# Kernel tuning notes

Measured on AMD Instinct MI355X. Metric: run time of the kernel, lower is better.

The kernel has to match this reference:

```python
import jax, jax.numpy as jnp
import numpy as np

N, E, C, NNZ, D = 100000, 50000, 2000, 1600000, 128


def _seg_mean(vals, idx, num):
    s = jax.ops.segment_sum(vals, idx, num_segments=num)
    cnt = jax.ops.segment_sum(jnp.ones((vals.shape[0],), vals.dtype), idx, num_segments=num)
    return s / jnp.maximum(cnt, 1.0)[:, None]


def _prelu(x, a):
    return jnp.where(x >= 0, x, a * x)


def setup_inputs() -> dict:
    key = jax.random.key(0)
    ks = jax.random.split(key, 32)
    x = jax.random.normal(ks[0], (N, D), jnp.float32)
    src = jax.random.randint(ks[1], (NNZ,), 0, N)
    dst = jax.random.randint(ks[2], (NNZ,), 0, E)
    hyperedge_index = jnp.stack([src, dst])
    hyperedge_component_index = jnp.stack([jnp.arange(E), jax.random.randint(ks[3], (E,), 0, C)])
    node_component_index = jnp.stack([jnp.arange(N), jax.random.randint(ks[4], (N,), 0, C)])
    inp = {
        'x': x,
        'hyperedge_index': hyperedge_index,
        'hyperedge_component_index': hyperedge_component_index,
        'node_component_index': node_component_index,
        'num_nodes': N, 'num_edges': E, 'num_components': C,
        'prelu_a': jnp.float32(0.25),
    }
    ki = 5
    for layer in range(2):
        for name in ['v2e', 'e2v', 'e2c', 'n2c']:
            inp[f'W_{name}_{layer}'] = jax.random.normal(ks[ki], (D, D), jnp.float32) / np.sqrt(D).astype(np.float32)
            inp[f'b_{name}_{layer}'] = jnp.zeros((D,), jnp.float32)
            ki += 1
    return inp


def reference(x, hyperedge_index, hyperedge_component_index, node_component_index,
              num_nodes, num_edges, num_components, prelu_a,
              W_v2e_0, b_v2e_0, W_e2v_0, b_e2v_0, W_e2c_0, b_e2c_0, W_n2c_0, b_n2c_0,
              W_v2e_1, b_v2e_1, W_e2v_1, b_e2v_1, W_e2c_1, b_e2c_1, W_n2c_1, b_n2c_1):
    Nn, Ne, Nc = num_nodes, num_edges, num_components
    # self-loop construction: node i joins fresh hyperedge Ne + i
    src = jnp.concatenate([hyperedge_index[0], jnp.arange(Nn)])
    dst = jnp.concatenate([hyperedge_index[1], jnp.arange(Ne, Ne + Nn)])
    E_tot = Ne + Nn
    he_e, he_c = hyperedge_component_index[0], hyperedge_component_index[1]
    nc_n, nc_c = node_component_index[0], node_component_index[1]

    def conv(h, Wv, bv, We, be, Wec, bec, Wnc, bnc):
        # node -> edge: transform, gather along incidences, scatter-mean to edges
        e = _prelu(_seg_mean((h @ Wv + bv)[src], dst, E_tot), prelu_a)
        # edge -> node
        n = _seg_mean((e @ We + be)[dst], src, Nn)
        # edge -> component  +  node -> component
        c = _prelu(_seg_mean((e @ Wec + bec)[he_e], he_c, Nc)
                   + _seg_mean((n @ Wnc + bnc)[nc_n], nc_c, Nc), prelu_a)
        return n, e, c

    n, e, c = conv(x, W_v2e_0, b_v2e_0, W_e2v_0, b_e2v_0, W_e2c_0, b_e2c_0, W_n2c_0, b_n2c_0)
    h = _prelu(n, prelu_a)
    n, e, c = conv(h, W_v2e_1, b_v2e_1, W_e2v_1, b_e2v_1, W_e2c_1, b_e2c_1, W_n2c_1, b_n2c_1)
    return _prelu(n, prelu_a), e[:Ne], c
```

## Files before the change

kernel.cpp:

```cpp
#include <hip/hip_runtime.h>
#include <hip/hip_bf16.h>

#define NN 100000
#define EE 50000
#define CC 2000
#define NNZ 1600000
#define DD 128
#define ET (EE + NN)

#define PB 800
#define CHUNK 2000
#define NBK 196
#define SCAP 12288

__device__ __forceinline__ float prelu(float x, float a) {
    return x >= 0.f ? x : a * x;
}

__device__ __forceinline__ float bf2f(unsigned short h) {
    return __uint_as_float(((unsigned int)h) << 16);
}
__device__ __forceinline__ unsigned short f2bf(float f) {
    unsigned int u = __float_as_uint(f);
    u = (u + 0x7fff + ((u >> 16) & 1)) >> 16;
    return (unsigned short)u;
}

struct alignas(16) us8 { ushort4 lo, hi; };

__global__ void comp_hist(const int* __restrict__ hec, const int* __restrict__ ncc,
                          int* __restrict__ c1cnt, int* __restrict__ c2cnt) {
    int i = blockIdx.x * blockDim.x + threadIdx.x;
    int stride = gridDim.x * blockDim.x;
    for (int k = i; k < EE; k += stride) atomicAdd(&c1cnt[hec[k]], 1);
    for (int k = i; k < NN; k += stride) atomicAdd(&c2cnt[ncc[k]], 1);
}

__global__ __launch_bounds__(256) void part_hist(const int* __restrict__ src,
                                                 const int* __restrict__ dst,
                                                 int* __restrict__ etot,
                                                 int* __restrict__ ntot) {
    __shared__ int he[NBK], hn[NBK];
    for (int i = threadIdx.x; i < NBK; i += 256) { he[i] = 0; hn[i] = 0; }
    __syncthreads();
    int b = blockIdx.x;
    int beg = b * CHUNK, end = min(beg + CHUNK, NNZ);
    for (int k = beg + threadIdx.x; k < end; k += 256) {
        atomicAdd(&he[dst[k] >> 8], 1);
        atomicAdd(&hn[src[k] >> 9], 1);
    }
    __syncthreads();
    for (int i = threadIdx.x; i < NBK; i += 256) {
        if (he[i]) atomicAdd(&etot[i], he[i]);
        if (hn[i]) atomicAdd(&ntot[i], hn[i]);
    }
}

__global__ __launch_bounds__(256) void scan_small(const int* __restrict__ etot,
        const int* __restrict__ ntot, int* __restrict__ ebase, int* __restrict__ nbase,
        int* __restrict__ ecur, int* __restrict__ ncur) {
    __shared__ int se[256], sn[256];
    int t = threadIdx.x;
    int ve = (t < NBK) ? etot[t] : 0;
    int vn = (t < NBK) ? ntot[t] : 0;
    se[t] = ve; sn[t] = vn;
    __syncthreads();
    for (int off = 1; off < 256; off <<= 1) {
        int ae = (t >= off) ? se[t - off] : 0;
        int an = (t >= off) ? sn[t - off] : 0;
        __syncthreads();
        se[t] += ae; sn[t] += an;
        __syncthreads();
    }
    if (t < NBK) {
        int be = se[t] - ve, bn = sn[t] - vn;
        ebase[t] = be; ecur[t] = be;
        nbase[t] = bn; ncur[t] = bn;
    }
    if (t == 0) { ebase[NBK] = NNZ; nbase[NBK] = NNZ; }
}

__global__ __launch_bounds__(256) void reorder_kernel(const int* __restrict__ src,
        const int* __restrict__ dst, int* __restrict__ ecur, int* __restrict__ ncur,
        int2* __restrict__ pe, int2* __restrict__ pn) {
    __shared__ int sS[CHUNK], sD[CHUNK];
    __shared__ int he[NBK], hn[NBK];
    __shared__ int beA[NBK], bnA[NBK];
    int b = blockIdx.x;
    int beg = b * CHUNK;
    int n = min(CHUNK, NNZ - beg);
    for (int i = threadIdx.x; i < NBK; i += 256) { he[i] = 0; hn[i] = 0; }
    for (int i = threadIdx.x; i < n; i += 256) {
        sS[i] = src[beg + i];
        sD[i] = dst[beg + i];
    }
    __syncthreads();
    for (int i = threadIdx.x; i < n; i += 256) {
        atomicAdd(&he[sD[i] >> 8], 1);
        atomicAdd(&hn[sS[i] >> 9], 1);
    }
    __syncthreads();
    for (int i = threadIdx.x; i < NBK; i += 256) {
        beA[i] = he[i] ? atomicAdd(&ecur[i], he[i]) : 0;
        bnA[i] = hn[i] ? atomicAdd(&ncur[i], hn[i]) : 0;
        he[i] = 0; hn[i] = 0;
    }
    __syncthreads();
    for (int i = threadIdx.x; i < n; i += 256) {
        int d = sD[i], s = sS[i];
        int bk = d >> 8;
        int p = beA[bk] + atomicAdd(&he[bk], 1);
        pe[p] = make_int2(d, s);
        bk = s >> 9;
        p = bnA[bk] + atomicAdd(&hn[bk], 1);
        pn[p] = make_int2(s, d);
    }
}

template <int W, int SHIFT>
__global__ __launch_bounds__(256) void bucket_scatter(const int2* __restrict__ pairs,
        const int* __restrict__ bases, int* __restrict__ ptr_excl,
        int* __restrict__ csr, int segn) {
    __shared__ int cnt[W];
    __shared__ int stage[SCAP];
    int b = blockIdx.x;
    int base = bases[b];
    int bend = bases[b + 1];
    int bsize = bend - base;

    for (int i = threadIdx.x; i < W; i += 256) cnt[i] = 0;
    __syncthreads();
    for (int k = base + threadIdx.x; k < bend; k += 256)
        atomicAdd(&cnt[pairs[k].x - (b << SHIFT)], 1);
    __syncthreads();

    int l0 = threadIdx.x, l1 = threadIdx.x + 256;
    int o0 = cnt[l0];
    int o1 = (W > 256) ? cnt[l1] : 0;
    for (int off = 1; off < W; off <<= 1) {
        int v0 = (l0 >= off) ? cnt[l0 - off] : 0;
        int v1 = 0;
        if (W > 256 && l1 >= off) v1 = cnt[l1 - off];
        __syncthreads();
        cnt[l0] += v0;
        if (W > 256) cnt[l1] += v1;
        __syncthreads();
    }
    int e0 = cnt[l0] - o0;
    int e1 = (W > 256) ? (cnt[l1] - o1) : 0;
    __syncthreads();
    cnt[l0] = base + e0;
    if (W > 256) cnt[l1] = base + e1;
    int g0 = (b << SHIFT) + l0;
    if (g0 < segn) ptr_excl[g0] = base + e0;
    if (W > 256) {
        int g1 = (b << SHIFT) + l1;
        if (g1 < segn) ptr_excl[g1] = base + e1;
    }
    if (b == NBK - 1 && threadIdx.x == 0) ptr_excl[segn] = NNZ;
    __syncthreads();

    bool fb = (bsize > SCAP);
    for (int k = base + threadIdx.x; k < bend; k += 256) {
        int2 pr = pairs[k];
        int pos = atomicAdd(&cnt[pr.x - (b << SHIFT)], 1);
        if (!fb) stage[pos - base] = pr.y;
        else     csr[pos] = pr.y;
    }
    __syncthreads();
    if (!fb)
        for (int t = threadIdx.x; t < bsize; t += 256) csr[base + t] = stage[t];
}

template <bool PRELU_IN, bool PRELU_OUT, bool OUT_BF16>
__global__ __launch_bounds__(256) void gemm128(
        const float* __restrict__ H, const float* __restrict__ W,
        const float* __restrict__ bias, void* __restrict__ outv,
        float* __restrict__ out2 ,
        const int* __restrict__ gate ,
        int M, const float* __restrict__ a_ptr) {
    __shared__ float Wl[128 * 128];
    for (int i = threadIdx.x; i < 4096; i += 256)
        ((float4*)Wl)[i] = ((const float4*)W)[i];
    float a = 0.f;
    if (PRELU_IN || PRELU_OUT) a = *a_ptr;
    __syncthreads();

    const int jc = threadIdx.x & 15;
    const int rg = threadIdx.x >> 4;
    const int j0 = jc * 8;
    const int row0 = blockIdx.x * 64 + rg * 4;

    float acc[4][8];
#pragma unroll
    for (int r = 0; r < 4; ++r)
#pragma unroll
        for (int c = 0; c < 8; ++c) acc[r][c] = 0.f;

    int rclamp[4];
#pragma unroll
    for (int r = 0; r < 4; ++r) {
        int row = row0 + r;
        rclamp[r] = row < M ? row : (M - 1);
    }

#pragma unroll 2
    for (int k0 = 0; k0 < 128; k0 += 4) {
        float hr[4][4];
#pragma unroll
        for (int r = 0; r < 4; ++r) {
            float4 v = *(const float4*)(H + (size_t)rclamp[r] * DD + k0);
            if (PRELU_IN) {
                v.x = prelu(v.x, a); v.y = prelu(v.y, a);
                v.z = prelu(v.z, a); v.w = prelu(v.w, a);
            }
            hr[r][0] = v.x; hr[r][1] = v.y; hr[r][2] = v.z; hr[r][3] = v.w;
        }
#pragma unroll
        for (int kk = 0; kk < 4; ++kk) {
            const float4 w0 = *(const float4*)&Wl[(k0 + kk) * 128 + j0];
            const float4 w1 = *(const float4*)&Wl[(k0 + kk) * 128 + j0 + 4];
#pragma unroll
            for (int r = 0; r < 4; ++r) {
                float h = hr[r][kk];
                acc[r][0] += h * w0.x; acc[r][1] += h * w0.y;
                acc[r][2] += h * w0.z; acc[r][3] += h * w0.w;
                acc[r][4] += h * w1.x; acc[r][5] += h * w1.y;
                acc[r][6] += h * w1.z; acc[r][7] += h * w1.w;
            }
        }
    }

    float bb[8];
#pragma unroll
    for (int c = 0; c < 8; ++c) bb[c] = bias[j0 + c];

#pragma unroll
    for (int r = 0; r < 4; ++r) {
        int row = row0 + r;
        if (row < M) {
            float g = 1.f;
            if (gate) g = (gate[row] > 0) ? 1.f : 0.f;
            float o[8];
#pragma unroll
            for (int c = 0; c < 8; ++c) o[c] = acc[r][c] + bb[c] * g;
            if (OUT_BF16) {
                us8 o8;
                o8.lo = make_ushort4(f2bf(o[0]), f2bf(o[1]), f2bf(o[2]), f2bf(o[3]));
                o8.hi = make_ushort4(f2bf(o[4]), f2bf(o[5]), f2bf(o[6]), f2bf(o[7]));
                *(us8*)((unsigned short*)outv + (size_t)row * DD + j0) = o8;
            } else {
                float* out = (float*)outv;
                *(float4*)(out + (size_t)row * DD + j0)     = make_float4(o[0], o[1], o[2], o[3]);
                *(float4*)(out + (size_t)row * DD + j0 + 4) = make_float4(o[4], o[5], o[6], o[7]);
            }
            if (PRELU_OUT) {
                *(float4*)(out2 + (size_t)row * DD + j0) =
                    make_float4(prelu(o[0], a), prelu(o[1], a), prelu(o[2], a), prelu(o[3], a));
                *(float4*)(out2 + (size_t)row * DD + j0 + 4) =
                    make_float4(prelu(o[4], a), prelu(o[5], a), prelu(o[6], a), prelu(o[7], a));
            }
        }
    }
}

__global__ __launch_bounds__(256) void edge_agg(const unsigned short* __restrict__ hv,
        const int* __restrict__ eptr, const int* __restrict__ ecsr,
        unsigned short* __restrict__ Eb, float* __restrict__ out_e,
        const float* __restrict__ a_ptr) {
    int j = blockIdx.x * 4 + (threadIdx.x >> 6);
    if (j >= EE) return;
    int lane = threadIdx.x & 63;
    int half = lane >> 5, l32 = lane & 31;
    int p0 = eptr[j], p1 = eptr[j + 1];
    float a = *a_ptr;
    float4 s = make_float4(0.f, 0.f, 0.f, 0.f);
    for (int p = p0 + half; p < p1; p += 2) {
        int row = ecsr[p];
        ushort4 v = *(const ushort4*)(hv + (size_t)row * DD + l32 * 4);
        s.x += bf2f(v.x); s.y += bf2f(v.y); s.z += bf2f(v.z); s.w += bf2f(v.w);
    }
    s.x += __shfl_xor(s.x, 32);
    s.y += __shfl_xor(s.y, 32);
    s.z += __shfl_xor(s.z, 32);
    s.w += __shfl_xor(s.w, 32);
    if (half == 0) {
        float inv = 1.0f / fmaxf((float)(p1 - p0), 1.0f);
        float4 o = make_float4(prelu(s.x * inv, a), prelu(s.y * inv, a),
                               prelu(s.z * inv, a), prelu(s.w * inv, a));
        *(ushort4*)(Eb + (size_t)j * DD + l32 * 4) =
            make_ushort4(f2bf(o.x), f2bf(o.y), f2bf(o.z), f2bf(o.w));
        if (out_e) *(float4*)(out_e + (size_t)j * DD + l32 * 4) = o;
    }
}

__global__ __launch_bounds__(256) void node_agg(const unsigned short* __restrict__ Eb,
        const unsigned short* __restrict__ hv, const int* __restrict__ nptr,
        const int* __restrict__ ncsr, float* __restrict__ nagg,
        const float* __restrict__ a_ptr) {
    int i = blockIdx.x * 4 + (threadIdx.x >> 6);
    if (i >= NN) return;
    int lane = threadIdx.x & 63;
    int half = lane >> 5, l32 = lane & 31;
    int p0 = nptr[i], p1 = nptr[i + 1];
    float a = *a_ptr;
    float4 s = make_float4(0.f, 0.f, 0.f, 0.f);
    if (half == 0) {
        ushort4 v = *(const ushort4*)(hv + (size_t)i * DD + l32 * 4);
        s.x = prelu(bf2f(v.x), a); s.y = prelu(bf2f(v.y), a);
        s.z = prelu(bf2f(v.z), a); s.w = prelu(bf2f(v.w), a);
    }
    for (int p = p0 + half; p < p1; p += 2) {
        int row = ncsr[p];
        ushort4 v = *(const ushort4*)(Eb + (size_t)row * DD + l32 * 4);
        s.x += bf2f(v.x); s.y += bf2f(v.y); s.z += bf2f(v.z); s.w += bf2f(v.w);
    }
    s.x += __shfl_xor(s.x, 32);
    s.y += __shfl_xor(s.y, 32);
    s.z += __shfl_xor(s.z, 32);
    s.w += __shfl_xor(s.w, 32);
    if (half == 0) {
        float inv = 1.0f / (float)(p1 - p0 + 1);
        *(float4*)(nagg + (size_t)i * DD + l32 * 4) =
            make_float4(s.x * inv, s.y * inv, s.z * inv, s.w * inv);
    }
}

__global__ void comp_scatter(const float* __restrict__ rows, const int* __restrict__ comp,
                             float* __restrict__ acc, int M) {
    int i = blockIdx.x * blockDim.x + threadIdx.x;
    int stride = gridDim.x * blockDim.x;
    int total = M * DD;
    for (int k = i; k < total; k += stride) {
        int r = k >> 7, d = k & 127;
        atomicAdd(&acc[(size_t)comp[r] * DD + d], rows[k]);
    }
}

__global__ void comp_scatter_bf16(const unsigned short* __restrict__ rows,
                                  const int* __restrict__ comp,
                                  float* __restrict__ acc, int M) {
    int i = blockIdx.x * blockDim.x + threadIdx.x;
    int stride = gridDim.x * blockDim.x;
    int total = M * DD;
    for (int k = i; k < total; k += stride) {
        int r = k >> 7, d = k & 127;
        atomicAdd(&acc[(size_t)comp[r] * DD + d], bf2f(rows[k]));
    }
}

__global__ void cmean(float* __restrict__ c1, float* __restrict__ c2,
                      const int* __restrict__ cnt1, const int* __restrict__ cnt2) {
    int k = blockIdx.x * blockDim.x + threadIdx.x;
    if (k >= CC * DD) return;
    int r = k >> 7;
    c1[k] *= 1.0f / (float)max(cnt1[r], 1);
    c2[k] *= 1.0f / (float)max(cnt2[r], 1);
}

__global__ void c_final(const float* __restrict__ c1, const float* __restrict__ c2,
                        float* __restrict__ out, const float* __restrict__ a_ptr) {
    float a = *a_ptr;
    int k = blockIdx.x * blockDim.x + threadIdx.x;
    if (k >= CC * DD) return;
    out[k] = prelu(c1[k] + c2[k], a);
}

extern "C" void kernel_launch(void* const* d_in, const int* in_sizes, int n_in,
                              void* d_out, int out_size, void* d_ws, size_t ws_size,
                              hipStream_t stream) {
    const float* x     = (const float*)d_in[0];
    const int* he_idx  = (const int*)d_in[1];
    const int* hcomp   = (const int*)d_in[2];
    const int* ncomp   = (const int*)d_in[3];
    const float* a_ptr = (const float*)d_in[7];

    const float *W[8], *B[8];
    for (int l = 0; l < 2; ++l)
        for (int m = 0; m < 4; ++m) {
            W[l * 4 + m] = (const float*)d_in[8 + l * 8 + m * 2];
            B[l * 4 + m] = (const float*)d_in[8 + l * 8 + m * 2 + 1];
        }

    const int* src = he_idx;
    const int* dst = he_idx + NNZ;
    const int* hec = hcomp + EE;
    const int* ncc = ncomp + NN;

    unsigned short* Hb = (unsigned short*)d_ws;
    unsigned short* Eb = Hb + (size_t)NN * DD;
    float* Ag = (float*)(Eb + (size_t)EE * DD);
    float* Nb = Ag + (size_t)NN * DD;
    float* zreg = Nb + (size_t)NN * DD;
    float* c1acc = zreg;
    float* c2acc = c1acc + CC * DD;
    int* c1cnt   = (int*)(c2acc + CC * DD);
    int* c2cnt   = c1cnt + CC;
    int* etot    = c2cnt + CC;
    int* ntot    = etot + NBK;
    size_t zbytes = (size_t)(2 * CC * DD + 2 * CC + 2 * NBK) * 4;
    int* ebase   = ntot + NBK;
    int* nbase   = ebase + (NBK + 1);
    int* ecur    = nbase + (NBK + 1);
    int* ncur    = ecur + NBK;
    float* c1row = (float*)(ncur + NBK);
    float* c2row = c1row + CC * DD;
    int* eptr    = (int*)(c2row + CC * DD);
    int* nptr    = eptr + (EE + 1);
    int* csr_e   = nptr + (NN + 1);
    int* csr_n   = csr_e + NNZ;

    int2* pairs_e = (int2*)Ag;
    int2* pairs_n = pairs_e + NNZ;

    float* out_n = (float*)d_out;
    float* out_e = out_n + (size_t)NN * DD;
    float* out_c = out_e + (size_t)EE * DD;

    hipMemsetAsync(zreg, 0, zbytes, stream);
    comp_hist<<<512, 256, 0, stream>>>(hec, ncc, c1cnt, c2cnt);
    part_hist<<<PB, 256, 0, stream>>>(src, dst, etot, ntot);
    scan_small<<<1, 256, 0, stream>>>(etot, ntot, ebase, nbase, ecur, ncur);
    reorder_kernel<<<PB, 256, 0, stream>>>(src, dst, ecur, ncur, pairs_e, pairs_n);
    bucket_scatter<256, 8><<<NBK, 256, 0, stream>>>(pairs_e, ebase, eptr, csr_e, EE);
    bucket_scatter<512, 9><<<NBK, 256, 0, stream>>>(pairs_n, nbase, nptr, csr_n, NN);

    const int gN  = (NN + 63) / 64;
    const int gC  = (CC + 63) / 64;
    const int gEA = EE / 4;
    const int gNA = NN / 4;

    gemm128<false, false, true><<<gN, 256, 0, stream>>>(x, W[0], B[0], Hb, nullptr, nullptr, NN, a_ptr);
    edge_agg<<<gEA, 256, 0, stream>>>(Hb, eptr, csr_e, Eb, nullptr, a_ptr);
    node_agg<<<gNA, 256, 0, stream>>>(Eb, Hb, nptr, csr_n, Ag, a_ptr);
    gemm128<false, false, false><<<gN, 256, 0, stream>>>(Ag, W[1], B[1], Nb, nullptr, nullptr, NN, a_ptr);

    gemm128<true, false, true><<<gN, 256, 0, stream>>>(Nb, W[4], B[4], Hb, nullptr, nullptr, NN, a_ptr);
    edge_agg<<<gEA, 256, 0, stream>>>(Hb, eptr, csr_e, Eb, out_e, a_ptr);
    node_agg<<<gNA, 256, 0, stream>>>(Eb, Hb, nptr, csr_n, Ag, a_ptr);
    gemm128<false, true, false><<<gN, 256, 0, stream>>>(Ag, W[5], B[5], Nb, out_n, nullptr, NN, a_ptr);

    comp_scatter_bf16<<<2048, 256, 0, stream>>>(Eb, hec, c1acc, EE);
    comp_scatter<<<2048, 256, 0, stream>>>(Nb, ncc, c2acc, NN);
    cmean<<<(CC * DD + 255) / 256, 256, 0, stream>>>(c1acc, c2acc, c1cnt, c2cnt);
    gemm128<false, false, false><<<gC, 256, 0, stream>>>(c1acc, W[6], B[6], c1row, nullptr, c1cnt, CC, a_ptr);
    gemm128<false, false, false><<<gC, 256, 0, stream>>>(c2acc, W[7], B[7], c2row, nullptr, c2cnt, CC, a_ptr);
    c_final<<<(CC * DD + 255) / 256, 256, 0, stream>>>(c1row, c2row, out_c, a_ptr);
}
```

Before: 1.020 ms.

## Slice bf16 feature tables per XCD so each die gathers from its own column slice

Hb is stored as 8 column slices of 16 features and Eb as 4 slices of 32 features. The edge and node aggregation grids are expanded so that block index mod 8 selects a slice, which maps each slice to one XCD. Each XCD then gathers only from its own slice, shrinking the working set per L2 and improving cache hit rates for the random gathers. The cost is more blocks, repeated reads of the CSR index per slice, narrower per-row loads, and extra shuffle reductions.

```diff
diff --git a/kernel.cpp b/kernel.cpp
--- a/kernel.cpp
+++ b/kernel.cpp
@@ -12,6 +12,7 @@
 #define CHUNK 2000
 #define NBK 196
 #define SCAP 12288
+
 
 __device__ __forceinline__ float prelu(float x, float a) {
     return x >= 0.f ? x : a * x;
@@ -248,7 +249,8 @@
                 us8 o8;
                 o8.lo = make_ushort4(f2bf(o[0]), f2bf(o[1]), f2bf(o[2]), f2bf(o[3]));
                 o8.hi = make_ushort4(f2bf(o[4]), f2bf(o[5]), f2bf(o[6]), f2bf(o[7]));
-                *(us8*)((unsigned short*)outv + (size_t)row * DD + j0) = o8;
+                *(us8*)((unsigned short*)outv +
+                        ((size_t)(j0 >> 4) * NN + row) * 16 + (j0 & 15)) = o8;
             } else {
                 float* out = (float*)outv;
                 *(float4*)(out + (size_t)row * DD + j0)     = make_float4(o[0], o[1], o[2], o[3]);
@@ -264,65 +266,83 @@
     }
 }
 
-__global__ __launch_bounds__(256) void edge_agg(const unsigned short* __restrict__ hv,
+__global__ __launch_bounds__(256) void edge_agg(const unsigned short* __restrict__ Hb,
         const int* __restrict__ eptr, const int* __restrict__ ecsr,
         unsigned short* __restrict__ Eb, float* __restrict__ out_e,
         const float* __restrict__ a_ptr) {
-    int j = blockIdx.x * 4 + (threadIdx.x >> 6);
-    if (j >= EE) return;
+    int b = blockIdx.x;
+    int e8 = b & 7;
+    int j  = (b >> 3) * 4 + (threadIdx.x >> 6);
     int lane = threadIdx.x & 63;
-    int half = lane >> 5, l32 = lane & 31;
+    int g = lane >> 2, l4 = lane & 3;
     int p0 = eptr[j], p1 = eptr[j + 1];
     float a = *a_ptr;
-    float4 s = make_float4(0.f, 0.f, 0.f, 0.f);
-    for (int p = p0 + half; p < p1; p += 2) {
+    float s0 = 0.f, s1 = 0.f, s2 = 0.f, s3 = 0.f;
+    const unsigned short* slice = Hb + (size_t)e8 * NN * 16;
+    for (int p = p0 + g; p < p1; p += 16) {
         int row = ecsr[p];
-        ushort4 v = *(const ushort4*)(hv + (size_t)row * DD + l32 * 4);
-        s.x += bf2f(v.x); s.y += bf2f(v.y); s.z += bf2f(v.z); s.w += bf2f(v.w);
-    }
-    s.x += __shfl_xor(s.x, 32);
-    s.y += __shfl_xor(s.y, 32);
-    s.z += __shfl_xor(s.z, 32);
-    s.w += __shfl_xor(s.w, 32);
-    if (half == 0) {
+        ushort4 v = *(const ushort4*)(slice + (size_t)row * 16 + l4 * 4);
+        s0 += bf2f(v.x); s1 += bf2f(v.y); s2 += bf2f(v.z); s3 += bf2f(v.w);
+    }
+#pragma unroll
+    for (int off = 4; off < 64; off <<= 1) {
+        s0 += __shfl_xor(s0, off); s1 += __shfl_xor(s1, off);
+        s2 += __shfl_xor(s2, off); s3 += __shfl_xor(s3, off);
+    }
+    if (g == 0) {
         float inv = 1.0f / fmaxf((float)(p1 - p0), 1.0f);
-        float4 o = make_float4(prelu(s.x * inv, a), prelu(s.y * inv, a),
-                               prelu(s.z * inv, a), prelu(s.w * inv, a));
-        *(ushort4*)(Eb + (size_t)j * DD + l32 * 4) =
+        float4 o = make_float4(prelu(s0 * inv, a), prelu(s1 * inv, a),
+                               prelu(s2 * inv, a), prelu(s3 * inv, a));
+        int q = e8 >> 1, hh = e8 & 1;
+        *(ushort4*)(Eb + ((size_t)q * EE + j) * 32 + hh * 16 + l4 * 4) =
             make_ushort4(f2bf(o.x), f2bf(o.y), f2bf(o.z), f2bf(o.w));
-        if (out_e) *(float4*)(out_e + (size_t)j * DD + l32 * 4) = o;
+        if (out_e)
+            *(float4*)(out_e + (size_t)j * DD + e8 * 16 + l4 * 4) = o;
     }
 }
 
 __global__ __launch_bounds__(256) void node_agg(const unsigned short* __restrict__ Eb,
-        const unsigned short* __restrict__ hv, const int* __restrict__ nptr,
-        const int* __restrict__ ncsr, float* __restrict__ nagg,
+        const unsigned short* __restrict__ Hb, const int* __restrict__ nptr,
+        const int* __restrict__ ncsr, float* __restrict__ Ag,
         const float* __restrict__ a_ptr) {
-    int i = blockIdx.x * 4 + (threadIdx.x >> 6);
-    if (i >= NN) return;
+    int b = blockIdx.x;
+    int xcd = b & 7;
+    int q = xcd >> 1, h = xcd & 1;
+    int i = (((b >> 3) * 2) + h) * 4 + (threadIdx.x >> 6);
     int lane = threadIdx.x & 63;
-    int half = lane >> 5, l32 = lane & 31;
+    int g = lane >> 2, l4 = lane & 3;
     int p0 = nptr[i], p1 = nptr[i + 1];
     float a = *a_ptr;
-    float4 s = make_float4(0.f, 0.f, 0.f, 0.f);
-    if (half == 0) {
-        ushort4 v = *(const ushort4*)(hv + (size_t)i * DD + l32 * 4);
-        s.x = prelu(bf2f(v.x), a); s.y = prelu(bf2f(v.y), a);
-        s.z = prelu(bf2f(v.z), a); s.w = prelu(bf2f(v.w), a);
-    }
-    for (int p = p0 + half; p < p1; p += 2) {
+    float s0=0.f,s1=0.f,s2=0.f,s3=0.f,s4=0.f,s5=0.f,s6=0.f,s7=0.f;
+    if (g == 0) {
+        const us8 v = *(const us8*)(Hb +
+            ((size_t)(2 * q + (l4 >> 1)) * NN + i) * 16 + (l4 & 1) * 8);
+        s0 = prelu(bf2f(v.lo.x), a); s1 = prelu(bf2f(v.lo.y), a);
+        s2 = prelu(bf2f(v.lo.z), a); s3 = prelu(bf2f(v.lo.w), a);
+        s4 = prelu(bf2f(v.hi.x), a); s5 = prelu(bf2f(v.hi.y), a);
+        s6 = prelu(bf2f(v.hi.z), a); s7 = prelu(bf2f(v.hi.w), a);
+    }
+    const unsigned short* slice = Eb + (size_t)q * EE * 32;
+    for (int p = p0 + g; p < p1; p += 16) {
         int row = ncsr[p];
-        ushort4 v = *(const ushort4*)(Eb + (size_t)row * DD + l32 * 4);
-        s.x += bf2f(v.x); s.y += bf2f(v.y); s.z += bf2f(v.z); s.w += bf2f(v.w);
-    }
-    s.x += __shfl_xor(s.x, 32);
-    s.y += __shfl_xor(s.y, 32);
-    s.z += __shfl_xor(s.z, 32);
-    s.w += __shfl_xor(s.w, 32);
-    if (half == 0) {
+        const us8 v = *(const us8*)(slice + (size_t)row * 32 + l4 * 8);
+        s0 += bf2f(v.lo.x); s1 += bf2f(v.lo.y);
+        s2 += bf2f(v.lo.z); s3 += bf2f(v.lo.w);
+        s4 += bf2f(v.hi.x); s5 += bf2f(v.hi.y);
+        s6 += bf2f(v.hi.z); s7 += bf2f(v.hi.w);
+    }
+#pragma unroll
+    for (int off = 4; off < 64; off <<= 1) {
+        s0 += __shfl_xor(s0, off); s1 += __shfl_xor(s1, off);
+        s2 += __shfl_xor(s2, off); s3 += __shfl_xor(s3, off);
+        s4 += __shfl_xor(s4, off); s5 += __shfl_xor(s5, off);
+        s6 += __shfl_xor(s6, off); s7 += __shfl_xor(s7, off);
+    }
+    if (g == 0) {
         float inv = 1.0f / (float)(p1 - p0 + 1);
-        *(float4*)(nagg + (size_t)i * DD + l32 * 4) =
-            make_float4(s.x * inv, s.y * inv, s.z * inv, s.w * inv);
+        float* w = Ag + (size_t)i * DD + q * 32 + l4 * 8;
+        *(float4*)(w)     = make_float4(s0 * inv, s1 * inv, s2 * inv, s3 * inv);
+        *(float4*)(w + 4) = make_float4(s4 * inv, s5 * inv, s6 * inv, s7 * inv);
     }
 }
 
@@ -337,7 +357,7 @@
     }
 }
 
-__global__ void comp_scatter_bf16(const unsigned short* __restrict__ rows,
+__global__ void comp_scatter_bf16(const unsigned short* __restrict__ Eb,
                                   const int* __restrict__ comp,
                                   float* __restrict__ acc, int M) {
     int i = blockIdx.x * blockDim.x + threadIdx.x;
@@ -345,7 +365,8 @@
     int total = M * DD;
     for (int k = i; k < total; k += stride) {
         int r = k >> 7, d = k & 127;
-        atomicAdd(&acc[(size_t)comp[r] * DD + d], bf2f(rows[k]));
+        unsigned short v = Eb[((size_t)(d >> 5) * EE + r) * 32 + (d & 31)];
+        atomicAdd(&acc[(size_t)comp[r] * DD + d], bf2f(v));
     }
 }
 
@@ -427,8 +448,8 @@
 
     const int gN  = (NN + 63) / 64;
     const int gC  = (CC + 63) / 64;
-    const int gEA = EE / 4;
-    const int gNA = NN / 4;
+    const int gEA = 8 * (EE / 4);
+    const int gNA = 8 * (NN / 8);
 
     gemm128<false, false, true><<<gN, 256, 0, stream>>>(x, W[0], B[0], Hb, nullptr, nullptr, NN, a_ptr);
     edge_agg<<<gEA, 256, 0, stream>>>(Hb, eptr, csr_e, Eb, nullptr, a_ptr);
```

Result: slower. 1.165 ms (+14.2%).
